# Performance work log

Hardware: AMD Instinct MI355X
Metric: run time of the kernel (lower is better)

Reference implementation:

```python
import jax, jax.numpy as jnp
import numpy as np

LOG_SIGMA0 = float(np.log(0.15))

def setup_inputs() -> dict:
    key = jax.random.key(0)
    k1, k2 = jax.random.split(key)
    B, S, O, D = 8, 4096, 1024, 3
    x = jax.random.uniform(k1, (B, S, D), dtype=jnp.float32)
    mus = jax.random.uniform(k2, (O, D), dtype=jnp.float32)
    log_sigmas = jnp.full((O,), LOG_SIGMA0, dtype=jnp.float32)
    return {"x": x, "mus": mus, "log_sigmas": log_sigmas}

def reference(x, mus, log_sigmas):
    # x: (B,S,D), mus: (O,D), log_sigmas: (O) -> y: (B,S,O)
    d_scaled = (x[:, :, None, :] - mus[None, None, :, :]) / jnp.exp(log_sigmas)[None, None, :, None]
    y = jnp.exp(-jnp.sum(d_scaled ** 2, axis=-1))
    # norm_basis=True
    y = y / jnp.sum(y, axis=-1, keepdims=True)
    return y
```

## Files before the change

kernel.cpp:

```cpp
#include <hip/hip_runtime.h>
#include <math.h>


#define O_DIM 1024
#define NPOINTS (8 * 4096)
#define BLOCKS 1024

__global__ __launch_bounds__(256, 4)
void GaussianRBF_83330955477629_kernel(const float* __restrict__ x,
                                       const float* __restrict__ mus,
                                       const float* __restrict__ log_sigmas,
                                       float* __restrict__ y) {
    const int lane  = threadIdx.x & 63;
    const int wave  = blockIdx.x * (blockDim.x >> 6) + (threadIdx.x >> 6);
    const int nwav  = gridDim.x * (blockDim.x >> 6);

    float mu0[16], mu1[16], mu2[16], w[16];
#pragma unroll
    for (int j = 0; j < 4; ++j) {
        const int o = j * 256 + lane * 4;
        const float4 m0 = *(const float4*)(mus + 3 * o);
        const float4 m1 = *(const float4*)(mus + 3 * o + 4);
        const float4 m2 = *(const float4*)(mus + 3 * o + 8);
        mu0[j*4+0] = m0.x; mu1[j*4+0] = m0.y; mu2[j*4+0] = m0.z;
        mu0[j*4+1] = m0.w; mu1[j*4+1] = m1.x; mu2[j*4+1] = m1.y;
        mu0[j*4+2] = m1.z; mu1[j*4+2] = m1.w; mu2[j*4+2] = m2.x;
        mu0[j*4+3] = m2.y; mu1[j*4+3] = m2.z; mu2[j*4+3] = m2.w;
        const float4 ls = *(const float4*)(log_sigmas + o);
        w[j*4+0] = __expf(-2.0f * ls.x);
        w[j*4+1] = __expf(-2.0f * ls.y);
        w[j*4+2] = __expf(-2.0f * ls.z);
        w[j*4+3] = __expf(-2.0f * ls.w);
    }

    for (int p = wave; p < NPOINTS; p += nwav) {
        const float x0 = x[p * 3 + 0];
        const float x1 = x[p * 3 + 1];
        const float x2 = x[p * 3 + 2];

        float yv[16];
        float s = 0.0f;
#pragma unroll
        for (int k = 0; k < 16; ++k) {
            const float d0 = x0 - mu0[k];
            const float d1 = x1 - mu1[k];
            const float d2 = x2 - mu2[k];
            const float q  = d0 * d0 + d1 * d1 + d2 * d2;
            const float v  = __expf(-w[k] * q);
            yv[k] = v;
            s += v;
        }
#pragma unroll
        for (int off = 32; off; off >>= 1) s += __shfl_xor(s, off, 64);
        const float r = 1.0f / s;

        float* yp = y + (size_t)p * O_DIM;
#pragma unroll
        for (int j = 0; j < 4; ++j) {
            float4 out;
            out.x = yv[j*4+0] * r;
            out.y = yv[j*4+1] * r;
            out.z = yv[j*4+2] * r;
            out.w = yv[j*4+3] * r;
            *(float4*)(yp + j * 256 + lane * 4) = out;
        }
    }
}

extern "C" void kernel_launch(void* const* d_in, const int* in_sizes, int n_in,
                              void* d_out, int out_size, void* d_ws, size_t ws_size,
                              hipStream_t stream) {
    const float* x  = (const float*)d_in[0];
    const float* mu = (const float*)d_in[1];
    const float* ls = (const float*)d_in[2];
    float* y = (float*)d_out;
    GaussianRBF_83330955477629_kernel<<<BLOCKS, 256, 0, stream>>>(x, mu, ls, y);
}
```

Baseline: 140.9 us.

## Double grid, process two points per wave iteration, use nontemporal stores

Doubles the block count and fully unrolls the per-wave point loop so each wave handles exactly four points, two interleaved at a time for more ILP. Output stores become nontemporal to keep the large streaming write from polluting cache, and the reciprocal uses the hardware rcp builtin instead of a divide. The loop bound is now hardcoded to the problem size, and the launch bound's occupancy hint is removed, which may change register allocation.

```diff
diff --git a/kernel.cpp b/kernel.cpp
--- a/kernel.cpp
+++ b/kernel.cpp
@@ -4,65 +4,77 @@
 
 #define O_DIM 1024
 #define NPOINTS (8 * 4096)
-#define BLOCKS 1024
+#define BLOCKS 2048
 
-__global__ __launch_bounds__(256, 4)
+typedef float vf4 __attribute__((ext_vector_type(4)));
+
+__global__ __launch_bounds__(256)
 void GaussianRBF_83330955477629_kernel(const float* __restrict__ x,
                                        const float* __restrict__ mus,
                                        const float* __restrict__ log_sigmas,
                                        float* __restrict__ y) {
-    const int lane  = threadIdx.x & 63;
-    const int wave  = blockIdx.x * (blockDim.x >> 6) + (threadIdx.x >> 6);
-    const int nwav  = gridDim.x * (blockDim.x >> 6);
+    const int lane = threadIdx.x & 63;
+    const int wave = blockIdx.x * 4 + (threadIdx.x >> 6);
+    const int nwav = BLOCKS * 4;
 
     float mu0[16], mu1[16], mu2[16], w[16];
 #pragma unroll
     for (int j = 0; j < 4; ++j) {
         const int o = j * 256 + lane * 4;
-        const float4 m0 = *(const float4*)(mus + 3 * o);
-        const float4 m1 = *(const float4*)(mus + 3 * o + 4);
-        const float4 m2 = *(const float4*)(mus + 3 * o + 8);
-        mu0[j*4+0] = m0.x; mu1[j*4+0] = m0.y; mu2[j*4+0] = m0.z;
-        mu0[j*4+1] = m0.w; mu1[j*4+1] = m1.x; mu2[j*4+1] = m1.y;
-        mu0[j*4+2] = m1.z; mu1[j*4+2] = m1.w; mu2[j*4+2] = m2.x;
-        mu0[j*4+3] = m2.y; mu1[j*4+3] = m2.z; mu2[j*4+3] = m2.w;
-        const float4 ls = *(const float4*)(log_sigmas + o);
-        w[j*4+0] = __expf(-2.0f * ls.x);
-        w[j*4+1] = __expf(-2.0f * ls.y);
-        w[j*4+2] = __expf(-2.0f * ls.z);
-        w[j*4+3] = __expf(-2.0f * ls.w);
+        const vf4 m0 = *(const vf4*)(mus + 3 * o);
+        const vf4 m1 = *(const vf4*)(mus + 3 * o + 4);
+        const vf4 m2 = *(const vf4*)(mus + 3 * o + 8);
+        mu0[j*4+0] = m0[0]; mu1[j*4+0] = m0[1]; mu2[j*4+0] = m0[2];
+        mu0[j*4+1] = m0[3]; mu1[j*4+1] = m1[0]; mu2[j*4+1] = m1[1];
+        mu0[j*4+2] = m1[2]; mu1[j*4+2] = m1[3]; mu2[j*4+2] = m2[0];
+        mu0[j*4+3] = m2[1]; mu1[j*4+3] = m2[2]; mu2[j*4+3] = m2[3];
+        const vf4 ls = *(const vf4*)(log_sigmas + o);
+        w[j*4+0] = __expf(-2.0f * ls[0]);
+        w[j*4+1] = __expf(-2.0f * ls[1]);
+        w[j*4+2] = __expf(-2.0f * ls[2]);
+        w[j*4+3] = __expf(-2.0f * ls[3]);
     }
 
-    for (int p = wave; p < NPOINTS; p += nwav) {
-        const float x0 = x[p * 3 + 0];
-        const float x1 = x[p * 3 + 1];
-        const float x2 = x[p * 3 + 2];
+#pragma unroll
+    for (int it = 0; it < 2; ++it) {
+        const int p0 = wave + (2 * it + 0) * nwav;
+        const int p1 = wave + (2 * it + 1) * nwav;
 
-        float yv[16];
-        float s = 0.0f;
+        const float a0 = x[p0 * 3 + 0], a1 = x[p0 * 3 + 1], a2 = x[p0 * 3 + 2];
+        const float b0 = x[p1 * 3 + 0], b1 = x[p1 * 3 + 1], b2 = x[p1 * 3 + 2];
+
+        float yv0[16], yv1[16];
+        float s0 = 0.0f, s1 = 0.0f;
 #pragma unroll
         for (int k = 0; k < 16; ++k) {
-            const float d0 = x0 - mu0[k];
-            const float d1 = x1 - mu1[k];
-            const float d2 = x2 - mu2[k];
-            const float q  = d0 * d0 + d1 * d1 + d2 * d2;
-            const float v  = __expf(-w[k] * q);
-            yv[k] = v;
-            s += v;
+            const float d0 = a0 - mu0[k], d1 = a1 - mu1[k], d2 = a2 - mu2[k];
+            const float e0 = b0 - mu0[k], e1 = b1 - mu1[k], e2 = b2 - mu2[k];
+            const float q0 = d0 * d0 + d1 * d1 + d2 * d2;
+            const float q1 = e0 * e0 + e1 * e1 + e2 * e2;
+            const float v0 = __expf(-w[k] * q0);
+            const float v1 = __expf(-w[k] * q1);
+            yv0[k] = v0; s0 += v0;
+            yv1[k] = v1; s1 += v1;
         }
 #pragma unroll
-        for (int off = 32; off; off >>= 1) s += __shfl_xor(s, off, 64);
-        const float r = 1.0f / s;
+        for (int off = 32; off; off >>= 1) {
+            s0 += __shfl_xor(s0, off, 64);
+            s1 += __shfl_xor(s1, off, 64);
+        }
+        const float r0 = __builtin_amdgcn_rcpf(s0);
+        const float r1 = __builtin_amdgcn_rcpf(s1);
 
-        float* yp = y + (size_t)p * O_DIM;
+        float* yp0 = y + (size_t)p0 * O_DIM;
+        float* yp1 = y + (size_t)p1 * O_DIM;
 #pragma unroll
         for (int j = 0; j < 4; ++j) {
-            float4 out;
-            out.x = yv[j*4+0] * r;
-            out.y = yv[j*4+1] * r;
-            out.z = yv[j*4+2] * r;
-            out.w = yv[j*4+3] * r;
-            *(float4*)(yp + j * 256 + lane * 4) = out;
+            vf4 o0, o1;
+            o0[0] = yv0[j*4+0] * r0; o0[1] = yv0[j*4+1] * r0;
+            o0[2] = yv0[j*4+2] * r0; o0[3] = yv0[j*4+3] * r0;
+            o1[0] = yv1[j*4+0] * r1; o1[1] = yv1[j*4+1] * r1;
+            o1[2] = yv1[j*4+2] * r1; o1[3] = yv1[j*4+3] * r1;
+            __builtin_nontemporal_store(o0, (vf4*)(yp0 + j * 256 + lane * 4));
+            __builtin_nontemporal_store(o1, (vf4*)(yp1 + j * 256 + lane * 4));
         }
     }
 }
```

Result: slower. 145.9 us (+3.6%).
